# Kernel optimization log

Measured on AMD Instinct MI355X. Metric: run time of the kernel, lower is better.

Reference implementation:

```python
import jax, jax.numpy as jnp
import numpy as np

B, T, H, S = 2, 2048, 16, 64
EMB = H * S  # 1024


def layer_norm(x, g, b, eps=1e-5):
    mu = jnp.mean(x, axis=-1, keepdims=True)
    var = jnp.var(x, axis=-1, keepdims=True)
    return (x - mu) * jax.lax.rsqrt(var + eps) * g + b


def setup_inputs() -> dict:
    key = jax.random.key(0)
    ks = jax.random.split(key, 12)
    sc = 0.02
    return {
        "x": jax.random.normal(ks[0], (B, T, EMB), dtype=jnp.float32),
        "Wkqv": jax.random.normal(ks[1], (S, 3 * S), dtype=jnp.float32) * sc,
        "Wproj": jax.random.normal(ks[2], (EMB, EMB), dtype=jnp.float32) * sc,
        "g1": jnp.ones((EMB,), jnp.float32),
        "b1": jnp.zeros((EMB,), jnp.float32),
        "W1": jax.random.normal(ks[3], (EMB, 4 * EMB), dtype=jnp.float32) * sc,
        "bff1": jnp.zeros((4 * EMB,), jnp.float32),
        "W2": jax.random.normal(ks[4], (4 * EMB, EMB), dtype=jnp.float32) * sc,
        "bff2": jnp.zeros((EMB,), jnp.float32),
        "g2": jnp.ones((EMB,), jnp.float32),
        "b2": jnp.zeros((EMB,), jnp.float32),
    }


def reference(x, Wkqv, Wproj, g1, b1, W1, bff1, W2, bff2, g2, b2):
    Bb, Tt, _ = x.shape
    xh = x.reshape(Bb, Tt, H, S)                     # [B,T,H,S]
    kqv = jnp.einsum('bths,sd->bthd', xh, Wkqv)      # [B,T,H,3S], shared per-head weight
    k, q, v = jnp.split(kqv, 3, axis=-1)             # note order: k, q, v
    scores = jnp.einsum('bihk,bjhk->bijh', q, k) / jnp.sqrt(jnp.float32(S))
    att = jax.nn.softmax(scores, axis=2)             # softmax over key dim j
    res = jnp.einsum('btih,bihs->bths', att, v).reshape(Bb, Tt, EMB)
    mha = res @ Wproj                                # Linear(emb, emb, bias=False)
    x = layer_norm(x + mha, g1, b1)
    h = jax.nn.gelu(x @ W1 + bff1, approximate=False)
    ff = h @ W2 + bff2
    return layer_norm(x + ff, g2, b2)
```

## Files before the change

### kernel.cpp

```cpp
#include <hip/hip_runtime.h>
#include <hip/hip_bf16.h>
#include <math.h>

#define B_ 2
#define T_ 2048
#define H_ 16
#define S_ 64
#define EMB 1024
#define FF 4096
#define BT (B_*T_)
#define ROWS (B_*T_*H_)

typedef __attribute__((ext_vector_type(8))) short s16x8;
typedef __attribute__((ext_vector_type(4))) float f32x4;

struct P4 { unsigned short* p[4]; };

__device__ __forceinline__ unsigned short f2b(float f) {
    return __builtin_bit_cast(unsigned short, __float2bfloat16(f));
}
__device__ __forceinline__ float b2f(short u) {
    return __builtin_bit_cast(float, ((unsigned int)(unsigned short)u) << 16);
}

__device__ __forceinline__ void gl_lds16(const void* g, void* l) {
    __builtin_amdgcn_global_load_lds(
        (const __attribute__((address_space(1))) void*)g,
        (__attribute__((address_space(3))) void*)l, 16, 0, 0);
}

__device__ __forceinline__ f32x4 mfma16(s16x8 a, s16x8 b, f32x4 c) {
    return __builtin_amdgcn_mfma_f32_16x16x32_bf16(a, b, c, 0, 0, 0);
}

#define WAIT_VM8 0x0F78
#define WAIT_VM0 0x0F70

__global__ __launch_bounds__(256) void kqv_kernel(const float* __restrict__ x,
        const unsigned short* __restrict__ Wqt, unsigned short* __restrict__ K,
        unsigned short* __restrict__ Q, unsigned short* __restrict__ V) {
    const int tid = threadIdx.x;
    const int w = tid >> 6, lane = tid & 63;
    const int l15 = lane & 15, quad = lane >> 4;
    const long r0 = (long)blockIdx.x * 128 + w * 32;

    s16x8 af[2][2];
    #pragma unroll
    for (int mt = 0; mt < 2; ++mt)
        #pragma unroll
        for (int ks = 0; ks < 2; ++ks) {
            const float* xp = x + (r0 + mt*16 + l15) * 64 + ks*32 + quad*8;
            const float4 v0 = *(const float4*)xp;
            const float4 v1 = *(const float4*)(xp + 4);
            s16x8 a;
            a[0] = (short)f2b(v0.x); a[1] = (short)f2b(v0.y);
            a[2] = (short)f2b(v0.z); a[3] = (short)f2b(v0.w);
            a[4] = (short)f2b(v1.x); a[5] = (short)f2b(v1.y);
            a[6] = (short)f2b(v1.z); a[7] = (short)f2b(v1.w);
            af[mt][ks] = a;
        }

    #pragma unroll
    for (int nt = 0; nt < 12; ++nt) {
        const s16x8 b0 = *(const s16x8*)&Wqt[(nt*16 + l15)*64 + quad*8];
        const s16x8 b1 = *(const s16x8*)&Wqt[(nt*16 + l15)*64 + 32 + quad*8];
        f32x4 acc[2] = {};
        #pragma unroll
        for (int mt = 0; mt < 2; ++mt) {
            acc[mt] = mfma16(af[mt][0], b0, acc[mt]);
            acc[mt] = mfma16(af[mt][1], b1, acc[mt]);
        }
        unsigned short* dst = (nt < 4) ? K : (nt < 8) ? Q : V;
        const int c0 = (nt & 3) * 16 + l15;
        #pragma unroll
        for (int mt = 0; mt < 2; ++mt)
            #pragma unroll
            for (int r = 0; r < 4; ++r)
                dst[(r0 + mt*16 + quad*4 + r) * 64 + c0] = f2b(acc[mt][r]);
    }
}

__global__ __launch_bounds__(256) void vt_kernel(const unsigned short* __restrict__ V,
        unsigned short* __restrict__ VT) {
    __shared__ unsigned short Ts[64][72];
    const int tid = threadIdx.x;
    const int tt = blockIdx.x, bh = blockIdx.y;
    const int b = bh >> 4, h = bh & 15;
    const long vbase = ((long)b * (T_*H_) + h) * 64;
    #pragma unroll
    for (int i = 0; i < 2; ++i) {
        const int id = i * 256 + tid;
        const int tr = id >> 3, dc = (id & 7) * 8;
        const s16x8 v = *(const s16x8*)&V[vbase + (long)(tt*64 + tr)*1024 + dc];
        *(s16x8*)&Ts[tr][dc] = v;
    }
    __syncthreads();
    #pragma unroll
    for (int i = 0; i < 2; ++i) {
        const int id = i * 256 + tid;
        const int d = id >> 3, tc = (id & 7) * 8;
        s16x8 o;
        #pragma unroll
        for (int j = 0; j < 8; ++j) o[j] = (short)Ts[tc + j][d];
        *(s16x8*)&VT[((long)bh*64 + d)*2048 + tt*64 + tc] = o;
    }
}

__global__ __launch_bounds__(64, 2) void attn_kernel(const unsigned short* __restrict__ Q,
        const unsigned short* __restrict__ K, const unsigned short* __restrict__ VT,
        unsigned short* __restrict__ res) {
    __shared__ __align__(16) unsigned short Kbuf[2][2][32*32];
    __shared__ __align__(16) unsigned short Vbuf[2][64*32];
    __shared__ __align__(16) unsigned short Ps[32*36];
    const int lane = threadIdx.x;
    const int l15 = lane & 15, quad = lane >> 4;
    const int bid = blockIdx.x;
    const int qt = bid & 63, bh = bid >> 6;
    const int b = bh >> 4, h = bh & 15;
    const long base = ((long)b * (T_*H_) + h) * 64;
    const unsigned short* Qp = Q + base;
    const unsigned short* Kp = K + base;
    const unsigned short* Vp = VT + (long)bh * 64 * 2048;
    const int q0 = qt * 32;

    s16x8 qf[2][2];
    #pragma unroll
    for (int qq = 0; qq < 2; ++qq)
        #pragma unroll
        for (int ks = 0; ks < 2; ++ks) {
            const s16x8 raw = *(const s16x8*)&Qp[(long)(q0 + qq*16 + l15)*1024 + ks*32 + quad*8];
            s16x8 q;
            #pragma unroll
            for (int j = 0; j < 8; ++j) q[j] = (short)f2b(b2f(raw[j]) * 0.125f);
            qf[qq][ks] = q;
        }

    s16x8 onef;
    #pragma unroll
    for (int j = 0; j < 8; ++j) onef[j] = (short)0x3F80;

    f32x4 oacc[2][4] = {};
    f32x4 lacc[2] = {};

    const int j16 = lane >> 2;
    const int c8  = (lane & 3) * 8;

    auto stage = [&](int bufi, int kt) {
        const unsigned short* kg = Kp + (long)(kt*32) * 1024;
        char* kl = (char*)&Kbuf[bufi][0][0];
        gl_lds16(kg + (long)j16*1024 + c8,           kl +    0 + lane*16);
        gl_lds16(kg + (long)(j16+16)*1024 + c8,      kl + 1024 + lane*16);
        gl_lds16(kg + (long)j16*1024 + 32 + c8,      kl + 2048 + lane*16);
        gl_lds16(kg + (long)(j16+16)*1024 + 32 + c8, kl + 3072 + lane*16);
        const unsigned short* vg = Vp + kt*32 + c8;
        char* vl = (char*)&Vbuf[bufi][0];
        gl_lds16(vg + (long)(j16     )*2048, vl +    0 + lane*16);
        gl_lds16(vg + (long)(j16 + 16)*2048, vl + 1024 + lane*16);
        gl_lds16(vg + (long)(j16 + 32)*2048, vl + 2048 + lane*16);
        gl_lds16(vg + (long)(j16 + 48)*2048, vl + 3072 + lane*16);
    };

    auto compute = [&](int bufi) {
        f32x4 sT[2][2] = {};
        #pragma unroll
        for (int ks = 0; ks < 2; ++ks)
            #pragma unroll
            for (int jt = 0; jt < 2; ++jt) {
                const s16x8 kf = *(const s16x8*)&Kbuf[bufi][ks][(jt*16 + l15)*32 + quad*8];
                sT[jt][0] = mfma16(kf, qf[0][ks], sT[jt][0]);
                sT[jt][1] = mfma16(kf, qf[1][ks], sT[jt][1]);
            }
        #pragma unroll
        for (int jt = 0; jt < 2; ++jt)
            #pragma unroll
            for (int qq = 0; qq < 2; ++qq) {
                uint2 pk;
                pk.x = (unsigned int)f2b(__expf(sT[jt][qq][0]))
                     | ((unsigned int)f2b(__expf(sT[jt][qq][1])) << 16);
                pk.y = (unsigned int)f2b(__expf(sT[jt][qq][2]))
                     | ((unsigned int)f2b(__expf(sT[jt][qq][3])) << 16);
                *(uint2*)&Ps[(qq*16 + l15)*36 + jt*16 + quad*4] = pk;
            }
        s16x8 pf[2];
        #pragma unroll
        for (int qq = 0; qq < 2; ++qq) {
            pf[qq] = *(const s16x8*)&Ps[(qq*16 + l15)*36 + quad*8];
            lacc[qq] = mfma16(pf[qq], onef, lacc[qq]);
        }
        #pragma unroll
        for (int nt = 0; nt < 4; ++nt) {
            const s16x8 vf = *(const s16x8*)&Vbuf[bufi][(nt*16 + l15)*32 + quad*8];
            oacc[0][nt] = mfma16(pf[0], vf, oacc[0][nt]);
            oacc[1][nt] = mfma16(pf[1], vf, oacc[1][nt]);
        }
    };

    stage(0, 0);
    for (int kt = 0; kt < 63; ++kt) {
        stage((kt + 1) & 1, kt + 1);
        __builtin_amdgcn_s_waitcnt(WAIT_VM8);
        __builtin_amdgcn_sched_barrier(0);
        compute(kt & 1);
    }
    __builtin_amdgcn_s_waitcnt(WAIT_VM0);
    __builtin_amdgcn_sched_barrier(0);
    compute(1);

    #pragma unroll
    for (int qq = 0; qq < 2; ++qq)
        #pragma unroll
        for (int r = 0; r < 4; ++r) {
            const float inv = 1.f / lacc[qq][r];
            const int t = q0 + qq*16 + quad*4 + r;
            #pragma unroll
            for (int nt = 0; nt < 4; ++nt)
                res[((long)(b*T_ + t))*EMB + h*64 + nt*16 + l15] =
                    f2b(oacc[qq][nt][r] * inv);
        }
}

__global__ __launch_bounds__(256) void gemm_gelu(const unsigned short* __restrict__ A,
        const unsigned short* __restrict__ Bt, const float* __restrict__ bias,
        unsigned short* __restrict__ C, int M, int N, int Kd) {
    __shared__ __align__(16) unsigned short As[2][128 * 32];
    __shared__ __align__(16) unsigned short Bs[2][128 * 32];
    const int tid = threadIdx.x;
    const int w = tid >> 6, lane = tid & 63;
    const int l15 = lane & 15, quad = lane >> 4;
    const int wm = w >> 1, wn = w & 1;
    const int bn = blockIdx.x, bm = blockIdx.y;
    const int sr = lane >> 2, skq = lane & 3;
    f32x4 acc[4][4] = {};
    const long arow = (long)(bm*128 + w*32 + sr);
    const long brow = (long)(bn*128 + w*32 + sr);

    auto stage = [&](int bi, int kt) {
        char* as = (char*)&As[bi][0];
        char* bs = (char*)&Bs[bi][0];
        gl_lds16(A  + (arow     )*Kd + kt + skq*8, as + (w*32     )*64 + lane*16);
        gl_lds16(A  + (arow + 16)*Kd + kt + skq*8, as + (w*32 + 16)*64 + lane*16);
        gl_lds16(Bt + (brow     )*Kd + kt + skq*8, bs + (w*32     )*64 + lane*16);
        gl_lds16(Bt + (brow + 16)*Kd + kt + skq*8, bs + (w*32 + 16)*64 + lane*16);
    };

    const int NT = Kd >> 5;
    stage(0, 0);
    __syncthreads();
    int bi = 0;
    for (int t = 0; t < NT; ++t) {
        if (t + 1 < NT) stage(bi ^ 1, (t + 1) * 32);
        s16x8 af[4], bf[4];
        #pragma unroll
        for (int mt = 0; mt < 4; ++mt)
            af[mt] = *(const s16x8*)&As[bi][(wm*64 + mt*16 + l15)*32 + quad*8];
        #pragma unroll
        for (int nt = 0; nt < 4; ++nt)
            bf[nt] = *(const s16x8*)&Bs[bi][(wn*64 + nt*16 + l15)*32 + quad*8];
        #pragma unroll
        for (int mt = 0; mt < 4; ++mt)
            #pragma unroll
            for (int nt = 0; nt < 4; ++nt)
                acc[mt][nt] = mfma16(af[mt], bf[nt], acc[mt][nt]);
        __syncthreads();
        bi ^= 1;
    }

    #pragma unroll
    for (int mt = 0; mt < 4; ++mt) {
        const int row0 = bm*128 + wm*64 + mt*16 + quad*4;
        #pragma unroll
        for (int nt = 0; nt < 4; ++nt) {
            const int col = bn*128 + wn*64 + nt*16 + l15;
            const float bv = bias[col];
            #pragma unroll
            for (int r = 0; r < 4; ++r) {
                float v = acc[mt][nt][r] + bv;
                v = 0.5f * v * (1.f + erff(v * 0.70710678118654752440f));
                C[(long)(row0 + r)*N + col] = f2b(v);
            }
        }
    }
}

__global__ __launch_bounds__(256) void gemm_splitk(const unsigned short* __restrict__ A,
        const unsigned short* __restrict__ Bt, P4 parts, int M, int N, int Kd, int Ks) {
    __shared__ __align__(16) unsigned short As[2][128 * 32];
    __shared__ __align__(16) unsigned short Bs[2][128 * 32];
    const int tid = threadIdx.x;
    const int w = tid >> 6, lane = tid & 63;
    const int l15 = lane & 15, quad = lane >> 4;
    const int wm = w >> 1, wn = w & 1;
    const int bn = blockIdx.x, bm = blockIdx.y, s = blockIdx.z;
    const int sr = lane >> 2, skq = lane & 3;
    f32x4 acc[4][4] = {};
    const long arow = (long)(bm*128 + w*32 + sr);
    const long brow = (long)(bn*128 + w*32 + sr);
    const int k0 = s * Ks;

    auto stage = [&](int bi, int kt) {
        char* as = (char*)&As[bi][0];
        char* bs = (char*)&Bs[bi][0];
        gl_lds16(A  + (arow     )*Kd + kt + skq*8, as + (w*32     )*64 + lane*16);
        gl_lds16(A  + (arow + 16)*Kd + kt + skq*8, as + (w*32 + 16)*64 + lane*16);
        gl_lds16(Bt + (brow     )*Kd + kt + skq*8, bs + (w*32     )*64 + lane*16);
        gl_lds16(Bt + (brow + 16)*Kd + kt + skq*8, bs + (w*32 + 16)*64 + lane*16);
    };

    const int NT = Ks >> 5;
    stage(0, k0);
    __syncthreads();
    int bi = 0;
    for (int t = 0; t < NT; ++t) {
        if (t + 1 < NT) stage(bi ^ 1, k0 + (t + 1) * 32);
        s16x8 af[4], bf[4];
        #pragma unroll
        for (int mt = 0; mt < 4; ++mt)
            af[mt] = *(const s16x8*)&As[bi][(wm*64 + mt*16 + l15)*32 + quad*8];
        #pragma unroll
        for (int nt = 0; nt < 4; ++nt)
            bf[nt] = *(const s16x8*)&Bs[bi][(wn*64 + nt*16 + l15)*32 + quad*8];
        #pragma unroll
        for (int mt = 0; mt < 4; ++mt)
            #pragma unroll
            for (int nt = 0; nt < 4; ++nt)
                acc[mt][nt] = mfma16(af[mt], bf[nt], acc[mt][nt]);
        __syncthreads();
        bi ^= 1;
    }

    unsigned short* Cp = parts.p[s];
    #pragma unroll
    for (int mt = 0; mt < 4; ++mt) {
        const int row0 = bm*128 + wm*64 + mt*16 + quad*4;
        #pragma unroll
        for (int nt = 0; nt < 4; ++nt) {
            const int col = bn*128 + wn*64 + nt*16 + l15;
            #pragma unroll
            for (int r = 0; r < 4; ++r)
                Cp[(long)(row0 + r)*N + col] = f2b(acc[mt][nt][r]);
        }
    }
}

template <int P, int XBF>
__global__ __launch_bounds__(256) void ln_kernel(const void* __restrict__ xa,
        P4 parts, const float* __restrict__ addb, const float* __restrict__ g,
        const float* __restrict__ bia, float* __restrict__ out,
        unsigned short* __restrict__ outb) {
    const int row = blockIdx.x;
    const int tid = threadIdx.x;
    float4 v;
    if (XBF) {
        const ushort4 u = ((const ushort4*)xa)[(long)row * (EMB/4) + tid];
        v.x = b2f((short)u.x); v.y = b2f((short)u.y);
        v.z = b2f((short)u.z); v.w = b2f((short)u.w);
    } else {
        v = ((const float4*)xa)[(long)row * (EMB/4) + tid];
    }
    #pragma unroll
    for (int p = 0; p < P; ++p) {
        const ushort4 u = ((const ushort4*)(parts.p[p] + (long)row * EMB))[tid];
        v.x += b2f((short)u.x); v.y += b2f((short)u.y);
        v.z += b2f((short)u.z); v.w += b2f((short)u.w);
    }
    if (addb) {
        const float4 ab = ((const float4*)addb)[tid];
        v.x += ab.x; v.y += ab.y; v.z += ab.z; v.w += ab.w;
    }
    float s = v.x + v.y + v.z + v.w;
    float ss = v.x * v.x + v.y * v.y + v.z * v.z + v.w * v.w;
    #pragma unroll
    for (int off = 32; off > 0; off >>= 1) {
        s += __shfl_down(s, off, 64);
        ss += __shfl_down(ss, off, 64);
    }
    __shared__ float ls[4], lss[4];
    __shared__ float mean_s, rstd_s;
    const int wid = tid >> 6, lane = tid & 63;
    if (lane == 0) { ls[wid] = s; lss[wid] = ss; }
    __syncthreads();
    if (tid == 0) {
        const float S0 = ls[0] + ls[1] + ls[2] + ls[3];
        const float S2 = lss[0] + lss[1] + lss[2] + lss[3];
        const float mean = S0 * (1.f / EMB);
        const float var = S2 * (1.f / EMB) - mean * mean;
        mean_s = mean;
        rstd_s = rsqrtf(var + 1e-5f);
    }
    __syncthreads();
    const float mean = mean_s, rstd = rstd_s;
    const float4 gg = ((const float4*)g)[tid];
    const float4 bb = ((const float4*)bia)[tid];
    float4 o;
    o.x = (v.x - mean) * rstd * gg.x + bb.x;
    o.y = (v.y - mean) * rstd * gg.y + bb.y;
    o.z = (v.z - mean) * rstd * gg.z + bb.z;
    o.w = (v.w - mean) * rstd * gg.w + bb.w;
    if (out) ((float4*)(out + (long)row * EMB))[tid] = o;
    if (outb) {
        unsigned short* ob = outb + (long)row * EMB + tid * 4;
        ob[0] = f2b(o.x); ob[1] = f2b(o.y); ob[2] = f2b(o.z); ob[3] = f2b(o.w);
    }
}

__global__ __launch_bounds__(256) void transp_all(const float* __restrict__ Wp,
        const float* __restrict__ W1, const float* __restrict__ W2,
        const float* __restrict__ Wq, unsigned short* __restrict__ Wpt,
        unsigned short* __restrict__ W1t, unsigned short* __restrict__ W2t,
        unsigned short* __restrict__ Wqt) {
    int id = blockIdx.x;
    const float* W; unsigned short* Wt; int Kd, N, ntx;
    if (id < 1024)      {            W = Wp; Wt = Wpt; Kd = 1024; N = 1024; ntx = 32; }
    else if (id < 5120) { id -= 1024; W = W1; Wt = W1t; Kd = 1024; N = 4096; ntx = 128; }
    else if (id < 9216) { id -= 5120; W = W2; Wt = W2t; Kd = 4096; N = 1024; ntx = 32; }
    else                { id -= 9216; W = Wq; Wt = Wqt; Kd = 64;   N = 192;  ntx = 6;  }
    __shared__ float Ts[32][33];
    const int tid = threadIdx.x;
    const int n0 = (id % ntx) * 32, k0 = (id / ntx) * 32;
    const int r = tid >> 3, c4 = (tid & 7) * 4;
    const float4 v = *(const float4*)&W[(long)(k0 + r) * N + n0 + c4];
    Ts[r][c4] = v.x; Ts[r][c4 + 1] = v.y; Ts[r][c4 + 2] = v.z; Ts[r][c4 + 3] = v.w;
    __syncthreads();
    #pragma unroll
    for (int i = 0; i < 4; ++i)
        Wt[(long)(n0 + r) * Kd + k0 + c4 + i] = f2b(Ts[c4 + i][r]);
}

extern "C" void kernel_launch(void* const* d_in, const int* in_sizes, int n_in,
                              void* d_out, int out_size, void* d_ws, size_t ws_size,
                              hipStream_t stream) {
    (void)in_sizes; (void)n_in; (void)out_size;
    const float* x     = (const float*)d_in[0];
    const float* Wkqv  = (const float*)d_in[1];
    const float* Wproj = (const float*)d_in[2];
    const float* g1    = (const float*)d_in[3];
    const float* b1    = (const float*)d_in[4];
    const float* W1    = (const float*)d_in[5];
    const float* bff1  = (const float*)d_in[6];
    const float* W2    = (const float*)d_in[7];
    const float* bff2  = (const float*)d_in[8];
    const float* g2    = (const float*)d_in[9];
    const float* b2    = (const float*)d_in[10];
    float* out = (float*)d_out;
    char* ws = (char*)d_ws;

    const size_t MB = 1u << 20;
    unsigned short* Qb   = (unsigned short*)(ws + 0 * MB);
    unsigned short* Kb   = (unsigned short*)(ws + 8 * MB);
    unsigned short* Vb   = (unsigned short*)(ws + 16 * MB);
    unsigned short* resb = (unsigned short*)(ws + 24 * MB);
    unsigned short* hb   = (unsigned short*)(ws + 8 * MB);
    unsigned short* VTb  = (unsigned short*)(ws + 40 * MB);
    unsigned short* mp0  = (unsigned short*)(ws + 40 * MB);
    unsigned short* mp1  = (unsigned short*)(ws + 48 * MB);
    unsigned short* x1b  = Qb;
    unsigned short* Wpt  = (unsigned short*)(ws + 72 * MB);
    unsigned short* W1t  = (unsigned short*)(ws + 74 * MB);
    unsigned short* W2t  = (unsigned short*)(ws + 82 * MB);
    unsigned short* Wqt  = (unsigned short*)(ws + 90 * MB);
    unsigned short* fp2  = (unsigned short*)(ws + 91 * MB);
    unsigned short* fp3  = (unsigned short*)(ws + 99 * MB);
    const bool big = ws_size >= 108 * MB;

    transp_all<<<dim3(9228), 256, 0, stream>>>(Wproj, W1, W2, Wkqv, Wpt, W1t, W2t, Wqt);

    kqv_kernel<<<dim3(ROWS/128), 256, 0, stream>>>(x, Wqt, Kb, Qb, Vb);
    vt_kernel<<<dim3(T_/64, B_*H_), 256, 0, stream>>>(Vb, VTb);
    attn_kernel<<<dim3(2048), 64, 0, stream>>>(Qb, Kb, VTb, resb);
    P4 mp; mp.p[0] = mp0; mp.p[1] = mp1; mp.p[2] = nullptr; mp.p[3] = nullptr;
    gemm_splitk<<<dim3(EMB/128, BT/128, 2), 256, 0, stream>>>(resb, Wpt, mp, BT, EMB, EMB, EMB/2);
    ln_kernel<2, 0><<<dim3(BT), 256, 0, stream>>>(x, mp, nullptr, g1, b1, nullptr, x1b);
    gemm_gelu<<<dim3(FF/128, BT/128), 256, 0, stream>>>(x1b, W1t, bff1, hb, BT, FF, EMB);
    if (big) {
        P4 fp; fp.p[0] = mp0; fp.p[1] = mp1; fp.p[2] = fp2; fp.p[3] = fp3;
        gemm_splitk<<<dim3(EMB/128, BT/128, 4), 256, 0, stream>>>(hb, W2t, fp, BT, EMB, FF, FF/4);
        ln_kernel<4, 1><<<dim3(BT), 256, 0, stream>>>(x1b, fp, bff2, g2, b2, out, nullptr);
    } else {
        P4 fp; fp.p[0] = mp0; fp.p[1] = mp1; fp.p[2] = nullptr; fp.p[3] = nullptr;
        gemm_splitk<<<dim3(EMB/128, BT/128, 2), 256, 0, stream>>>(hb, W2t, fp, BT, EMB, FF, FF/2);
        ln_kernel<2, 1><<<dim3(BT), 256, 0, stream>>>(x1b, fp, bff2, g2, b2, out, nullptr);
    }
}
```

Baseline: 352.6 us.

## Share K/V tiles across four waves per block in attention kernel

The attention kernel now runs four waves per block, each handling 32 queries of a 128-query group, and they share the double-buffered K and V tiles in LDS. Each wave issues a quarter of the global-to-LDS loads, so each K/V tile is fetched once per four query tiles instead of once per query tile. The cost is two workgroup barriers per key tile, which can stall waves and reduce the latency hiding previously provided by independent single-wave blocks. The grid also shrinks from 2048 to 512 blocks.

Result: slower. 362.7 us (+2.9%).

```diff
diff --git a/kernel.cpp b/kernel.cpp
--- a/kernel.cpp
+++ b/kernel.cpp
@@ -34,6 +34,7 @@
 }
 
 #define WAIT_VM8 0x0F78
+#define WAIT_VM2 0x0F72
 #define WAIT_VM0 0x0F70
 
 __global__ __launch_bounds__(256) void kqv_kernel(const float* __restrict__ x,
@@ -106,22 +107,24 @@
     }
 }
 
-__global__ __launch_bounds__(64, 2) void attn_kernel(const unsigned short* __restrict__ Q,
+__global__ __launch_bounds__(256) void attn_kernel(const unsigned short* __restrict__ Q,
         const unsigned short* __restrict__ K, const unsigned short* __restrict__ VT,
         unsigned short* __restrict__ res) {
     __shared__ __align__(16) unsigned short Kbuf[2][2][32*32];
     __shared__ __align__(16) unsigned short Vbuf[2][64*32];
-    __shared__ __align__(16) unsigned short Ps[32*36];
-    const int lane = threadIdx.x;
+    __shared__ __align__(16) unsigned short Ps[4][32*36];
+    const int tid = threadIdx.x;
+    const int wid = tid >> 6, lane = tid & 63;
     const int l15 = lane & 15, quad = lane >> 4;
     const int bid = blockIdx.x;
-    const int qt = bid & 63, bh = bid >> 6;
+    const int qg = bid & 15, bh = bid >> 4;
     const int b = bh >> 4, h = bh & 15;
     const long base = ((long)b * (T_*H_) + h) * 64;
     const unsigned short* Qp = Q + base;
     const unsigned short* Kp = K + base;
     const unsigned short* Vp = VT + (long)bh * 64 * 2048;
-    const int q0 = qt * 32;
+    const int q0 = qg * 128 + wid * 32;
+    unsigned short* ps = &Ps[wid][0];
 
     s16x8 qf[2][2];
     #pragma unroll
@@ -146,18 +149,28 @@
     const int c8  = (lane & 3) * 8;
 
     auto stage = [&](int bufi, int kt) {
+        char* kl = (char*)&Kbuf[bufi][0][0];
+        char* vl = (char*)&Vbuf[bufi][0];
         const unsigned short* kg = Kp + (long)(kt*32) * 1024;
-        char* kl = (char*)&Kbuf[bufi][0][0];
-        gl_lds16(kg + (long)j16*1024 + c8,           kl +    0 + lane*16);
-        gl_lds16(kg + (long)(j16+16)*1024 + c8,      kl + 1024 + lane*16);
-        gl_lds16(kg + (long)j16*1024 + 32 + c8,      kl + 2048 + lane*16);
-        gl_lds16(kg + (long)(j16+16)*1024 + 32 + c8, kl + 3072 + lane*16);
         const unsigned short* vg = Vp + kt*32 + c8;
-        char* vl = (char*)&Vbuf[bufi][0];
-        gl_lds16(vg + (long)(j16     )*2048, vl +    0 + lane*16);
-        gl_lds16(vg + (long)(j16 + 16)*2048, vl + 1024 + lane*16);
-        gl_lds16(vg + (long)(j16 + 32)*2048, vl + 2048 + lane*16);
-        gl_lds16(vg + (long)(j16 + 48)*2048, vl + 3072 + lane*16);
+        switch (wid) {
+        case 0:
+            gl_lds16(kg + (long)j16*1024 + c8,           kl +    0 + lane*16);
+            gl_lds16(kg + (long)(j16+16)*1024 + c8,      kl + 1024 + lane*16);
+            break;
+        case 1:
+            gl_lds16(kg + (long)j16*1024 + 32 + c8,      kl + 2048 + lane*16);
+            gl_lds16(kg + (long)(j16+16)*1024 + 32 + c8, kl + 3072 + lane*16);
+            break;
+        case 2:
+            gl_lds16(vg + (long)(j16     )*2048, vl +    0 + lane*16);
+            gl_lds16(vg + (long)(j16 + 16)*2048, vl + 1024 + lane*16);
+            break;
+        default:
+            gl_lds16(vg + (long)(j16 + 32)*2048, vl + 2048 + lane*16);
+            gl_lds16(vg + (long)(j16 + 48)*2048, vl + 3072 + lane*16);
+            break;
+        }
     };
 
     auto compute = [&](int bufi) {
@@ -179,12 +192,12 @@
                      | ((unsigned int)f2b(__expf(sT[jt][qq][1])) << 16);
                 pk.y = (unsigned int)f2b(__expf(sT[jt][qq][2]))
                      | ((unsigned int)f2b(__expf(sT[jt][qq][3])) << 16);
-                *(uint2*)&Ps[(qq*16 + l15)*36 + jt*16 + quad*4] = pk;
+                *(uint2*)&ps[(qq*16 + l15)*36 + jt*16 + quad*4] = pk;
             }
         s16x8 pf[2];
         #pragma unroll
         for (int qq = 0; qq < 2; ++qq) {
-            pf[qq] = *(const s16x8*)&Ps[(qq*16 + l15)*36 + quad*8];
+            pf[qq] = *(const s16x8*)&ps[(qq*16 + l15)*36 + quad*8];
             lacc[qq] = mfma16(pf[qq], onef, lacc[qq]);
         }
         #pragma unroll
@@ -198,11 +211,15 @@
     stage(0, 0);
     for (int kt = 0; kt < 63; ++kt) {
         stage((kt + 1) & 1, kt + 1);
-        __builtin_amdgcn_s_waitcnt(WAIT_VM8);
+        __builtin_amdgcn_s_waitcnt(WAIT_VM2);
+        __builtin_amdgcn_s_barrier();
         __builtin_amdgcn_sched_barrier(0);
         compute(kt & 1);
+        __builtin_amdgcn_s_barrier();
+        __builtin_amdgcn_sched_barrier(0);
     }
     __builtin_amdgcn_s_waitcnt(WAIT_VM0);
+    __builtin_amdgcn_s_barrier();
     __builtin_amdgcn_sched_barrier(0);
     compute(1);
 
@@ -466,7 +483,7 @@
 
     kqv_kernel<<<dim3(ROWS/128), 256, 0, stream>>>(x, Wqt, Kb, Qb, Vb);
     vt_kernel<<<dim3(T_/64, B_*H_), 256, 0, stream>>>(Vb, VTb);
-    attn_kernel<<<dim3(2048), 64, 0, stream>>>(Qb, Kb, VTb, resb);
+    attn_kernel<<<dim3(512), 256, 0, stream>>>(Qb, Kb, VTb, resb);
     P4 mp; mp.p[0] = mp0; mp.p[1] = mp1; mp.p[2] = nullptr; mp.p[3] = nullptr;
     gemm_splitk<<<dim3(EMB/128, BT/128, 2), 256, 0, stream>>>(resb, Wpt, mp, BT, EMB, EMB, EMB/2);
     ln_kernel<2, 0><<<dim3(BT), 256, 0, stream>>>(x, mp, nullptr, g1, b1, nullptr, x1b);
```
